# Kernel tuning notes

Measured on AMD Instinct MI355X. Metric: run time of the kernel, lower is better.

## Reference

```python
import jax, jax.numpy as jnp
import numpy as np

B, N, DIM = 2, 2048, 2048
H, HD = 16, 128
EPS = 1e-5


def rmsnorm(x, w, eps=EPS):
    return x * jax.lax.rsqrt(jnp.mean(x * x, axis=-1, keepdims=True) + eps) * w


def rope(x, fr, fi):
    # x: [B, N, H, D]; fr/fi: [B, N, D//2] -> broadcast over heads
    x2 = x.reshape(*x.shape[:-1], HD // 2, 2)  # [B,N,H,D/2,2]
    x0, x1 = x2[..., 0], x2[..., 1]
    fr = fr[:, :, None, :]
    fi = fi[:, :, None, :]
    o0 = x0 * fr - x1 * fi
    o1 = x0 * fi + x1 * fr
    return jnp.stack([o0, o1], axis=-1).reshape(x.shape)


def setup_inputs() -> dict:
    key = jax.random.key(0)
    ks = jax.random.split(key, 7)
    s = 1.0 / np.sqrt(DIM)
    return {
        "x": jax.random.normal(ks[0], (B, N, DIM), jnp.float32),
        "freqs_real": jax.random.normal(ks[1], (B, N, HD // 2), jnp.float32),
        "freqs_imag": jax.random.normal(ks[2], (B, N, HD // 2), jnp.float32),
        "w_qkv": jax.random.normal(ks[3], (DIM, 3 * H * HD), jnp.float32) * s,
        "w_out": jax.random.normal(ks[4], (H * HD, DIM), jnp.float32) * s,
        "q_norm_w": jnp.ones((HD,), jnp.float32),
        "k_norm_w": jnp.ones((HD,), jnp.float32),
    }


def reference(x, freqs_real, freqs_imag, w_qkv, w_out, q_norm_w, k_norm_w):
    qkv = (x @ w_qkv).reshape(B, N, 3, H, HD)
    q, k, v = qkv[:, :, 0], qkv[:, :, 1], qkv[:, :, 2]  # [B,N,H,D]
    q = rmsnorm(q, q_norm_w)
    k = rmsnorm(k, k_norm_w)
    q = rope(q, freqs_real, freqs_imag)
    k = rope(k, freqs_real, freqs_imag)
    scale = 1.0 / np.sqrt(HD)
    scores = jnp.einsum("bqhd,bkhd->bhqk", q, k) * scale
    attn = jax.nn.softmax(scores, axis=-1)
    out = jnp.einsum("bhqk,bkhd->bqhd", attn, v).reshape(B, N, H * HD)
    return out @ w_out
```

## Files before the change

kernel.cpp:

```cpp
#include <hip/hip_runtime.h>
#include <hip/hip_bf16.h>
#include <stdint.h>

#define B_    2
#define N_    2048
#define DIM_  2048
#define H_    16
#define HD_   128
#define NH3   6144
#define ROWS  4096
#define EPS_  1e-5f

typedef unsigned short u16;
typedef __bf16 bf16x8 __attribute__((ext_vector_type(8)));
typedef float  f32x4  __attribute__((ext_vector_type(4)));

__device__ inline f32x4 mfma16(bf16x8 a, bf16x8 b, f32x4 c) {
  return __builtin_amdgcn_mfma_f32_16x16x32_bf16(a, b, c, 0, 0, 0);
}

__device__ inline u16 f2bf(float f) {
  union { float f; uint32_t u; } v; v.f = f;
  uint32_t u = v.u;
  return (u16)((u + 0x7fffu + ((u >> 16) & 1u)) >> 16);
}
__device__ inline float bf2f(u16 u) {
  union { uint32_t u; float f; } v; v.u = ((uint32_t)u) << 16;
  return v.f;
}

__device__ inline void gload_lds16(const void* g, void* l) {
  __builtin_amdgcn_global_load_lds(
      (const __attribute__((address_space(1))) void*)g,
      (__attribute__((address_space(3))) void*)l, 16, 0, 0);
}

__global__ __launch_bounds__(256) void cvt_f32_bf16(const float* __restrict__ in,
                                                    u16* __restrict__ out, int n) {
  int i = (blockIdx.x * 256 + threadIdx.x) * 4;
  if (i >= n) return;
  float4 v = *(const float4*)&in[i];
  ushort4 o;
  o.x = f2bf(v.x); o.y = f2bf(v.y); o.z = f2bf(v.z); o.w = f2bf(v.w);
  *(ushort4*)&out[i] = o;
}

__global__ __launch_bounds__(256) void transpose_cvt(const float* __restrict__ in,
                                                     u16* __restrict__ out,
                                                     int R, int C) {
  __shared__ float tile[32][33];
  int tc = blockIdx.x * 32, tr = blockIdx.y * 32;
  int tx = threadIdx.x, ty = threadIdx.y;
  #pragma unroll
  for (int i = 0; i < 4; ++i)
    tile[ty + i*8][tx] = in[(size_t)(tr + ty + i*8) * C + tc + tx];
  __syncthreads();
  #pragma unroll
  for (int i = 0; i < 4; ++i)
    out[(size_t)(tc + ty + i*8) * R + tr + tx] = f2bf(tile[tx][ty + i*8]);
}

__global__ __launch_bounds__(256) void v_transpose(const u16* __restrict__ qkv,
                                                   u16* __restrict__ vt) {
  __shared__ u16 lT[64][130];
  int bh = blockIdx.y, n0 = blockIdx.x * 64;
  int b = bh >> 4, h = bh & 15;
  int t = threadIdx.x;
  const u16* Vb = qkv + (size_t)b * N_ * NH3 + 4096 + h * HD_;
  #pragma unroll
  for (int i = 0; i < 16; ++i) {
    int chunk = i * 256 + t;
    int n = chunk >> 6, dc = chunk & 63;
    *(ushort2*)&lT[n][dc*2] = *(const ushort2*)&Vb[(size_t)(n0+n)*NH3 + dc*2];
  }
  __syncthreads();
  u16* vo = vt + (size_t)bh * HD_ * N_;
  #pragma unroll
  for (int i = 0; i < 4; ++i) {
    int chunk = i * 256 + t;
    int d = chunk >> 3, nc = chunk & 7;
    ushort4 a, bq;
    a.x = lT[nc*8+0][d]; a.y = lT[nc*8+1][d]; a.z = lT[nc*8+2][d]; a.w = lT[nc*8+3][d];
    bq.x = lT[nc*8+4][d]; bq.y = lT[nc*8+5][d]; bq.z = lT[nc*8+6][d]; bq.w = lT[nc*8+7][d];
    u16* dst = &vo[(size_t)d * N_ + n0 + nc*8];
    *(ushort4*)dst = a;
    *(ushort4*)(dst+4) = bq;
  }
}

template <bool OUT_BF16>
__global__ __launch_bounds__(256) void gemm_bt(const u16* __restrict__ A,
                                               const u16* __restrict__ Bt,
                                               void* __restrict__ Cv,
                                               int M, int N, int K) {
  __shared__ u16 lA[128][64];
  __shared__ u16 lB[128][64];
  int m0 = blockIdx.x * 128, n0 = blockIdx.y * 128;
  int t = threadIdx.x;
  int wave = t >> 6, lane = t & 63;
  int wr = wave >> 1, wc = wave & 1;
  int lhi = lane >> 4, llo = lane & 15;
  int lrow = lane >> 3, lcol = lane & 7;
  f32x4 acc[4][4] = {};

  for (int k0 = 0; k0 < K; k0 += 64) {
    __syncthreads();
    #pragma unroll
    for (int i = 0; i < 4; ++i) {
      int chunk = i * 4 + wave;
      int row = chunk * 8 + lrow;
      gload_lds16(&A[(size_t)(m0+row)*K + k0 + lcol*8], &lA[chunk*8][0]);
      gload_lds16(&Bt[(size_t)(n0+row)*K + k0 + lcol*8], &lB[chunk*8][0]);
    }
    __syncthreads();
    #pragma unroll
    for (int kk = 0; kk < 2; ++kk) {
      bf16x8 af[4], bfr[4];
      #pragma unroll
      for (int mi = 0; mi < 4; ++mi)
        af[mi] = *(const bf16x8*)&lA[wr*64 + mi*16 + llo][kk*32 + lhi*8];
      #pragma unroll
      for (int ni = 0; ni < 4; ++ni)
        bfr[ni] = *(const bf16x8*)&lB[wc*64 + ni*16 + llo][kk*32 + lhi*8];
      #pragma unroll
      for (int mi = 0; mi < 4; ++mi)
        #pragma unroll
        for (int ni = 0; ni < 4; ++ni)
          acc[mi][ni] = mfma16(af[mi], bfr[ni], acc[mi][ni]);
    }
  }
  #pragma unroll
  for (int mi = 0; mi < 4; ++mi)
    #pragma unroll
    for (int ni = 0; ni < 4; ++ni)
      #pragma unroll
      for (int r = 0; r < 4; ++r) {
        int row = m0 + wr*64 + mi*16 + lhi*4 + r;
        int col = n0 + wc*64 + ni*16 + llo;
        float v = acc[mi][ni][r];
        if constexpr (OUT_BF16) ((u16*)Cv)[(size_t)row*N + col] = f2bf(v);
        else                    ((float*)Cv)[(size_t)row*N + col] = v;
      }
}

__global__ __launch_bounds__(256) void norm_rope(u16* __restrict__ qkv,
                                                 const float* __restrict__ fr,
                                                 const float* __restrict__ fi,
                                                 const float* __restrict__ qw,
                                                 const float* __restrict__ kw) {
  int gw = (blockIdx.x * 256 + threadIdx.x) >> 6;
  int lane = threadIdx.x & 63;
  int row = gw >> 4, h = gw & 15;
  size_t base = (size_t)row * NH3 + h * HD_;
  ushort2 qp = *(ushort2*)&qkv[base + 2*lane];
  ushort2 kp = *(ushort2*)&qkv[base + 2048 + 2*lane];
  float q0 = bf2f(qp.x), q1 = bf2f(qp.y);
  float k0 = bf2f(kp.x), k1 = bf2f(kp.y);
  float sq = q0*q0 + q1*q1;
  float sk = k0*k0 + k1*k1;
  #pragma unroll
  for (int off = 1; off < 64; off <<= 1) {
    sq += __shfl_xor(sq, off);
    sk += __shfl_xor(sk, off);
  }
  float rq = rsqrtf(sq * (1.0f/128.0f) + EPS_);
  float rk = rsqrtf(sk * (1.0f/128.0f) + EPS_);
  float wq0 = qw[2*lane], wq1 = qw[2*lane+1];
  float wk0 = kw[2*lane], wk1 = kw[2*lane+1];
  q0 *= rq * wq0; q1 *= rq * wq1;
  k0 *= rk * wk0; k1 *= rk * wk1;
  float fre = fr[(size_t)row*64 + lane], fim = fi[(size_t)row*64 + lane];
  float qo0 = q0*fre - q1*fim, qo1 = q0*fim + q1*fre;
  float ko0 = k0*fre - k1*fim, ko1 = k0*fim + k1*fre;
  const float SC = 0.08838834764831845f;
  qo0 *= SC; qo1 *= SC;
  ushort2 qo, ko;
  qo.x = f2bf(qo0); qo.y = f2bf(qo1);
  ko.x = f2bf(ko0); ko.y = f2bf(ko1);
  *(ushort2*)&qkv[base + 2*lane] = qo;
  *(ushort2*)&qkv[base + 2048 + 2*lane] = ko;
}

__global__ __launch_bounds__(256) void attn(const u16* __restrict__ qkv,
                                            const u16* __restrict__ vt,
                                            u16* __restrict__ out) {
  int bh = blockIdx.y;
  int b = bh >> 4, h = bh & 15;
  int q0 = blockIdx.x * 128;
  int t = threadIdx.x, wave = t >> 6, lane = t & 63;
  int lhi = lane >> 4, llo = lane & 15;

  __shared__ u16 lK[64][136];
  __shared__ u16 lVt[128][72];
  __shared__ u16 lP[4][32][72];

  const u16* Qb  = qkv + (size_t)b * N_ * NH3 + h * HD_;
  const u16* Kb  = Qb + 2048;
  const u16* Vtb = vt + (size_t)bh * HD_ * N_;

  bf16x8 qf[2][4];
  #pragma unroll
  for (int pi = 0; pi < 2; ++pi) {
    const u16* qrow = Qb + (size_t)(q0 + wave*32 + pi*16 + llo) * NH3;
    #pragma unroll
    for (int kk = 0; kk < 4; ++kk)
      qf[pi][kk] = *(const bf16x8*)&qrow[kk*32 + lhi*8];
  }

  f32x4 o[2][8] = {};
  float m[2][4], l[2][4];
  #pragma unroll
  for (int pi = 0; pi < 2; ++pi)
    #pragma unroll
    for (int r = 0; r < 4; ++r) { m[pi][r] = -1e30f; l[pi][r] = 0.f; }

  for (int kv0 = 0; kv0 < N_; kv0 += 64) {
    __syncthreads();
    #pragma unroll
    for (int i = 0; i < 4; ++i) {
      int chunk = i*256 + t;
      int row = chunk >> 4, kc = chunk & 15;
      *(int4*)&lK[row][kc*8] = *(const int4*)&Kb[(size_t)(kv0+row)*NH3 + kc*8];
    }
    #pragma unroll
    for (int i = 0; i < 4; ++i) {
      int chunk = i*256 + t;
      int d = chunk >> 3, kvc = chunk & 7;
      *(int4*)&lVt[d][kvc*8] = *(const int4*)&Vtb[(size_t)d*N_ + kv0 + kvc*8];
    }
    __syncthreads();

    f32x4 S[2][4];
    #pragma unroll
    for (int pi = 0; pi < 2; ++pi)
      #pragma unroll
      for (int j = 0; j < 4; ++j) S[pi][j] = f32x4{0.f,0.f,0.f,0.f};
    #pragma unroll
    for (int j = 0; j < 4; ++j)
      #pragma unroll
      for (int kk = 0; kk < 4; ++kk) {
        bf16x8 kf = *(const bf16x8*)&lK[j*16 + llo][kk*32 + lhi*8];
        S[0][j] = mfma16(qf[0][kk], kf, S[0][j]);
        S[1][j] = mfma16(qf[1][kk], kf, S[1][j]);
      }

    float sc[2][4];
    #pragma unroll
    for (int pi = 0; pi < 2; ++pi)
      #pragma unroll
      for (int r = 0; r < 4; ++r) {
        float rm = fmaxf(fmaxf(S[pi][0][r], S[pi][1][r]), fmaxf(S[pi][2][r], S[pi][3][r]));
        #pragma unroll
        for (int off = 1; off < 16; off <<= 1) rm = fmaxf(rm, __shfl_xor(rm, off));
        float mnew = fmaxf(m[pi][r], rm);
        sc[pi][r] = __expf(m[pi][r] - mnew);
        m[pi][r] = mnew;
      }
    #pragma unroll
    for (int pi = 0; pi < 2; ++pi)
      #pragma unroll
      for (int r = 0; r < 4; ++r) {
        float s0 = __expf(S[pi][0][r] - m[pi][r]);
        float s1 = __expf(S[pi][1][r] - m[pi][r]);
        float s2 = __expf(S[pi][2][r] - m[pi][r]);
        float s3 = __expf(S[pi][3][r] - m[pi][r]);
        S[pi][0][r] = s0; S[pi][1][r] = s1; S[pi][2][r] = s2; S[pi][3][r] = s3;
        float rs = s0 + s1 + s2 + s3;
        #pragma unroll
        for (int off = 1; off < 16; off <<= 1) rs += __shfl_xor(rs, off);
        l[pi][r] = l[pi][r]*sc[pi][r] + rs;
      }
    #pragma unroll
    for (int pi = 0; pi < 2; ++pi)
      #pragma unroll
      for (int d = 0; d < 8; ++d)
        #pragma unroll
        for (int r = 0; r < 4; ++r) o[pi][d][r] *= sc[pi][r];

    #pragma unroll
    for (int pi = 0; pi < 2; ++pi)
      #pragma unroll
      for (int j = 0; j < 4; ++j)
        #pragma unroll
        for (int r = 0; r < 4; ++r) {
          int prow = pi*16 + lhi*4 + r;
          int pcol = (j*16 + llo) ^ (lhi << 3);
          lP[wave][prow][pcol] = f2bf(S[pi][j][r]);
        }

    #pragma unroll
    for (int kk = 0; kk < 2; ++kk) {
      bf16x8 pf[2];
      #pragma unroll
      for (int pi = 0; pi < 2; ++pi) {
        int prow = pi*16 + llo;
        int pcol = (kk*32 + lhi*8) ^ (((llo >> 2) & 3) << 3);
        pf[pi] = *(const bf16x8*)&lP[wave][prow][pcol];
      }
      #pragma unroll
      for (int d = 0; d < 8; ++d) {
        bf16x8 vf = *(const bf16x8*)&lVt[d*16 + llo][kk*32 + lhi*8];
        o[0][d] = mfma16(pf[0], vf, o[0][d]);
        o[1][d] = mfma16(pf[1], vf, o[1][d]);
      }
    }
  }

  #pragma unroll
  for (int pi = 0; pi < 2; ++pi)
    #pragma unroll
    for (int r = 0; r < 4; ++r) l[pi][r] = 1.0f / l[pi][r];
  #pragma unroll
  for (int pi = 0; pi < 2; ++pi)
    #pragma unroll
    for (int d = 0; d < 8; ++d)
      #pragma unroll
      for (int r = 0; r < 4; ++r) {
        size_t row = (size_t)b*N_ + q0 + wave*32 + pi*16 + lhi*4 + r;
        out[row*2048 + h*HD_ + d*16 + llo] = f2bf(o[pi][d][r] * l[pi][r]);
      }
}

extern "C" void kernel_launch(void* const* d_in, const int* in_sizes, int n_in,
                              void* d_out, int out_size, void* d_ws, size_t ws_size,
                              hipStream_t stream) {
  const float* x    = (const float*)d_in[0];
  const float* fr   = (const float*)d_in[1];
  const float* fi   = (const float*)d_in[2];
  const float* wqkv = (const float*)d_in[3];
  const float* wout = (const float*)d_in[4];
  const float* qw   = (const float*)d_in[5];
  const float* kw   = (const float*)d_in[6];
  float* out = (float*)d_out;

  char* ws = (char*)d_ws;
  const size_t SZ_XB    = (size_t)ROWS * DIM_ * 2;
  const size_t SZ_WQKVT = (size_t)NH3  * DIM_ * 2;
  const size_t SZ_WOUTT = (size_t)DIM_ * DIM_ * 2;
  u16* xb    = (u16*)ws;
  u16* wqkvT = (u16*)(ws + SZ_XB);
  u16* woutT = (u16*)(ws + SZ_XB + SZ_WQKVT);
  u16* qkv   = (u16*)(ws + SZ_XB + SZ_WQKVT + SZ_WOUTT);
  u16* vtb   = xb;
  u16* attno = wqkvT;

  cvt_f32_bf16<<<(ROWS*DIM_/4 + 255)/256, 256, 0, stream>>>(x, xb, ROWS*DIM_);
  transpose_cvt<<<dim3(NH3/32, DIM_/32), dim3(32, 8), 0, stream>>>(wqkv, wqkvT, DIM_, NH3);
  transpose_cvt<<<dim3(DIM_/32, DIM_/32), dim3(32, 8), 0, stream>>>(wout, woutT, DIM_, DIM_);
  gemm_bt<true ><<<dim3(ROWS/128, NH3/128), 256, 0, stream>>>(xb, wqkvT, qkv, ROWS, NH3, DIM_);
  norm_rope<<<ROWS*H_/4, 256, 0, stream>>>(qkv, fr, fi, qw, kw);
  v_transpose<<<dim3(N_/64, B_*H_), 256, 0, stream>>>(qkv, vtb);
  attn<<<dim3(N_/128, B_*H_), 256, 0, stream>>>(qkv, vtb, attno);
  gemm_bt<false><<<dim3(ROWS/128, DIM_/128), 256, 0, stream>>>(attno, woutT, out, ROWS, DIM_, DIM_);
}
```

Measured before the change: 563.4 us.

## Remap blocks across XCDs and compute transposed S tiles in attention

The GEMM and attention kernels now launch 1D grids and remap block IDs so that consecutive logical tiles land on the same XCD, which should improve L2 reuse of shared A/B or K/V tiles. The attention kernel also computes S transposed (K as the A operand), so each lane owns one query row. Softmax max and sum then need only two cross-lane shuffles instead of four-step reductions per row, and P can be written to LDS as packed 4-element stores without swizzling. The cost is extra shuffles to broadcast rescale factors, and the unswizzled P layout may cause LDS bank conflicts.

```diff
diff --git a/kernel.cpp b/kernel.cpp
--- a/kernel.cpp
+++ b/kernel.cpp
@@ -95,7 +95,10 @@
                                                int M, int N, int K) {
   __shared__ u16 lA[128][64];
   __shared__ u16 lB[128][64];
-  int m0 = blockIdx.x * 128, n0 = blockIdx.y * 128;
+  int per = gridDim.x >> 3;
+  int nid = (blockIdx.x & 7) * per + (blockIdx.x >> 3);
+  int MB = M >> 7;
+  int m0 = (nid % MB) * 128, n0 = (nid / MB) * 128;
   int t = threadIdx.x;
   int wave = t >> 6, lane = t & 63;
   int wr = wave >> 1, wc = wave & 1;
@@ -184,9 +187,10 @@
 __global__ __launch_bounds__(256) void attn(const u16* __restrict__ qkv,
                                             const u16* __restrict__ vt,
                                             u16* __restrict__ out) {
-  int bh = blockIdx.y;
+  int nid = (blockIdx.x & 7) * 64 + (blockIdx.x >> 3);
+  int bh = nid >> 4;
   int b = bh >> 4, h = bh & 15;
-  int q0 = blockIdx.x * 128;
+  int q0 = (nid & 15) * 128;
   int t = threadIdx.x, wave = t >> 6, lane = t & 63;
   int lhi = lane >> 4, llo = lane & 15;
 
@@ -208,11 +212,8 @@
   }
 
   f32x4 o[2][8] = {};
-  float m[2][4], l[2][4];
-  #pragma unroll
-  for (int pi = 0; pi < 2; ++pi)
-    #pragma unroll
-    for (int r = 0; r < 4; ++r) { m[pi][r] = -1e30f; l[pi][r] = 0.f; }
+  float m_own[2] = {-1e30f, -1e30f};
+  float l_own[2] = {0.f, 0.f};
 
   for (int kv0 = 0; kv0 < N_; kv0 += 64) {
     __syncthreads();
@@ -230,73 +231,73 @@
     }
     __syncthreads();
 
-    f32x4 S[2][4];
+    f32x4 St[2][4];
     #pragma unroll
     for (int pi = 0; pi < 2; ++pi)
       #pragma unroll
-      for (int j = 0; j < 4; ++j) S[pi][j] = f32x4{0.f,0.f,0.f,0.f};
+      for (int j = 0; j < 4; ++j) St[pi][j] = f32x4{0.f,0.f,0.f,0.f};
     #pragma unroll
     for (int j = 0; j < 4; ++j)
       #pragma unroll
       for (int kk = 0; kk < 4; ++kk) {
         bf16x8 kf = *(const bf16x8*)&lK[j*16 + llo][kk*32 + lhi*8];
-        S[0][j] = mfma16(qf[0][kk], kf, S[0][j]);
-        S[1][j] = mfma16(qf[1][kk], kf, S[1][j]);
-      }
-
-    float sc[2][4];
-    #pragma unroll
-    for (int pi = 0; pi < 2; ++pi)
-      #pragma unroll
-      for (int r = 0; r < 4; ++r) {
-        float rm = fmaxf(fmaxf(S[pi][0][r], S[pi][1][r]), fmaxf(S[pi][2][r], S[pi][3][r]));
-        #pragma unroll
-        for (int off = 1; off < 16; off <<= 1) rm = fmaxf(rm, __shfl_xor(rm, off));
-        float mnew = fmaxf(m[pi][r], rm);
-        sc[pi][r] = __expf(m[pi][r] - mnew);
-        m[pi][r] = mnew;
-      }
-    #pragma unroll
-    for (int pi = 0; pi < 2; ++pi)
-      #pragma unroll
-      for (int r = 0; r < 4; ++r) {
-        float s0 = __expf(S[pi][0][r] - m[pi][r]);
-        float s1 = __expf(S[pi][1][r] - m[pi][r]);
-        float s2 = __expf(S[pi][2][r] - m[pi][r]);
-        float s3 = __expf(S[pi][3][r] - m[pi][r]);
-        S[pi][0][r] = s0; S[pi][1][r] = s1; S[pi][2][r] = s2; S[pi][3][r] = s3;
-        float rs = s0 + s1 + s2 + s3;
-        #pragma unroll
-        for (int off = 1; off < 16; off <<= 1) rs += __shfl_xor(rs, off);
-        l[pi][r] = l[pi][r]*sc[pi][r] + rs;
-      }
-    #pragma unroll
-    for (int pi = 0; pi < 2; ++pi)
-      #pragma unroll
-      for (int d = 0; d < 8; ++d)
-        #pragma unroll
-        for (int r = 0; r < 4; ++r) o[pi][d][r] *= sc[pi][r];
-
-    #pragma unroll
-    for (int pi = 0; pi < 2; ++pi)
+        St[0][j] = mfma16(kf, qf[0][kk], St[0][j]);
+        St[1][j] = mfma16(kf, qf[1][kk], St[1][j]);
+      }
+
+    float scb[2][4];
+    #pragma unroll
+    for (int pi = 0; pi < 2; ++pi) {
+      float mx = -1e30f;
+      #pragma unroll
+      for (int j = 0; j < 4; ++j) {
+        float a = fmaxf(fmaxf(St[pi][j][0], St[pi][j][1]),
+                        fmaxf(St[pi][j][2], St[pi][j][3]));
+        mx = fmaxf(mx, a);
+      }
+      mx = fmaxf(mx, __shfl_xor(mx, 16));
+      mx = fmaxf(mx, __shfl_xor(mx, 32));
+      float mnew = fmaxf(m_own[pi], mx);
+      float sc = __expf(m_own[pi] - mnew);
+      m_own[pi] = mnew;
+      float rs = 0.f;
       #pragma unroll
       for (int j = 0; j < 4; ++j)
         #pragma unroll
         for (int r = 0; r < 4; ++r) {
-          int prow = pi*16 + lhi*4 + r;
-          int pcol = (j*16 + llo) ^ (lhi << 3);
-          lP[wave][prow][pcol] = f2bf(S[pi][j][r]);
+          float p = __expf(St[pi][j][r] - mnew);
+          St[pi][j][r] = p;
+          rs += p;
         }
+      rs += __shfl_xor(rs, 16);
+      rs += __shfl_xor(rs, 32);
+      l_own[pi] = l_own[pi] * sc + rs;
+      #pragma unroll
+      for (int r = 0; r < 4; ++r) scb[pi][r] = __shfl(sc, lhi*4 + r, 16);
+    }
+    #pragma unroll
+    for (int pi = 0; pi < 2; ++pi)
+      #pragma unroll
+      for (int d = 0; d < 8; ++d)
+        #pragma unroll
+        for (int r = 0; r < 4; ++r) o[pi][d][r] *= scb[pi][r];
+
+    #pragma unroll
+    for (int pi = 0; pi < 2; ++pi)
+      #pragma unroll
+      for (int j = 0; j < 4; ++j) {
+        union { ushort4 u; __bf16 hv[4]; } pw;
+        #pragma unroll
+        for (int r = 0; r < 4; ++r) pw.hv[r] = (__bf16)St[pi][j][r];
+        *(ushort4*)&lP[wave][pi*16 + llo][j*16 + lhi*4] = pw.u;
+      }
 
     #pragma unroll
     for (int kk = 0; kk < 2; ++kk) {
       bf16x8 pf[2];
       #pragma unroll
-      for (int pi = 0; pi < 2; ++pi) {
-        int prow = pi*16 + llo;
-        int pcol = (kk*32 + lhi*8) ^ (((llo >> 2) & 3) << 3);
-        pf[pi] = *(const bf16x8*)&lP[wave][prow][pcol];
-      }
+      for (int pi = 0; pi < 2; ++pi)
+        pf[pi] = *(const bf16x8*)&lP[wave][pi*16 + llo][kk*32 + lhi*8];
       #pragma unroll
       for (int d = 0; d < 8; ++d) {
         bf16x8 vf = *(const bf16x8*)&lVt[d*16 + llo][kk*32 + lhi*8];
@@ -306,10 +307,12 @@
     }
   }
 
+  float linv[2][4];
   #pragma unroll
   for (int pi = 0; pi < 2; ++pi)
     #pragma unroll
-    for (int r = 0; r < 4; ++r) l[pi][r] = 1.0f / l[pi][r];
+    for (int r = 0; r < 4; ++r)
+      linv[pi][r] = 1.0f / __shfl(l_own[pi], lhi*4 + r, 16);
   #pragma unroll
   for (int pi = 0; pi < 2; ++pi)
     #pragma unroll
@@ -317,7 +320,7 @@
       #pragma unroll
       for (int r = 0; r < 4; ++r) {
         size_t row = (size_t)b*N_ + q0 + wave*32 + pi*16 + lhi*4 + r;
-        out[row*2048 + h*HD_ + d*16 + llo] = f2bf(o[pi][d][r] * l[pi][r]);
+        out[row*2048 + h*HD_ + d*16 + llo] = f2bf(o[pi][d][r] * linv[pi][r]);
       }
 }
 
@@ -347,9 +350,9 @@
   cvt_f32_bf16<<<(ROWS*DIM_/4 + 255)/256, 256, 0, stream>>>(x, xb, ROWS*DIM_);
   transpose_cvt<<<dim3(NH3/32, DIM_/32), dim3(32, 8), 0, stream>>>(wqkv, wqkvT, DIM_, NH3);
   transpose_cvt<<<dim3(DIM_/32, DIM_/32), dim3(32, 8), 0, stream>>>(wout, woutT, DIM_, DIM_);
-  gemm_bt<true ><<<dim3(ROWS/128, NH3/128), 256, 0, stream>>>(xb, wqkvT, qkv, ROWS, NH3, DIM_);
+  gemm_bt<true ><<<(ROWS/128)*(NH3/128), 256, 0, stream>>>(xb, wqkvT, qkv, ROWS, NH3, DIM_);
   norm_rope<<<ROWS*H_/4, 256, 0, stream>>>(qkv, fr, fi, qw, kw);
   v_transpose<<<dim3(N_/64, B_*H_), 256, 0, stream>>>(qkv, vtb);
-  attn<<<dim3(N_/128, B_*H_), 256, 0, stream>>>(qkv, vtb, attno);
-  gemm_bt<false><<<dim3(ROWS/128, DIM_/128), 256, 0, stream>>>(attno, woutT, out, ROWS, DIM_, DIM_);
-}
+  attn<<<(N_/128)*(B_*H_), 256, 0, stream>>>(qkv, vtb, attno);
+  gemm_bt<false><<<(ROWS/128)*(DIM_/128), 256, 0, stream>>>(attno, woutT, out, ROWS, DIM_, DIM_);
+}
```

After: 551.6 us. 2.1% less time.
